# Performance work log

Hardware: AMD Instinct MI355X
Metric: run time of the kernel (lower is better)

## Reference

```python
import jax, jax.numpy as jnp
import numpy as np

DELTA_COEFF = 1.0
CLAMP_MIN = 1e-3  # hardcoded in original clamp(min=0.001)


def setup_inputs() -> dict:
    key = jax.random.key(0)
    k1, k2, k3 = jax.random.split(key, 3)
    B, N, F_in, F_out = 2, 1024, 128, 64
    x = jax.random.normal(k1, (B, N, F_in), dtype=jnp.float32)
    adj = jax.random.uniform(k2, (B, N, N), dtype=jnp.float32)
    weight = jax.random.normal(k3, (F_in, F_out), dtype=jnp.float32) * (1.0 / np.sqrt(F_in))
    bias = jnp.zeros((F_out,), dtype=jnp.float32)
    return {"x": x, "adj": adj, "weight": weight, "bias": bias}


def reference(x, adj, weight, bias):
    # x: [B,N,F_in], adj: [B,N,N]
    x = x @ weight  # [B,N,F_out]
    B, N, _ = adj.shape
    # pairwise L1 distance: [B,N,N]
    abs_diff = jnp.sum(jnp.abs(x[:, :, None, :] - x[:, None, :, :]), axis=-1)
    mod_adj = adj / jnp.maximum(abs_diff, CLAMP_MIN)
    deg = jnp.sum(mod_adj, axis=-1)  # [B,N]
    # Laplacian L = D - A~ ; then I - delta * L
    lap = jnp.zeros_like(mod_adj).at[:, jnp.arange(N), jnp.arange(N)].set(deg) - mod_adj
    mod = jnp.eye(N, dtype=x.dtype) - DELTA_COEFF * lap
    out = jnp.matmul(mod, x) + bias
    return out
```

## Files before the change

### kernel.cpp

```cpp
#include <hip/hip_runtime.h>
#include <hip/hip_fp16.h>


#define JS 16
#define HSTR 72

typedef _Float16 half8_t __attribute__((ext_vector_type(8)));
typedef _Float16 h2_t    __attribute__((ext_vector_type(2)));
typedef float    f32x4_t __attribute__((ext_vector_type(4)));

static __device__ __forceinline__ h2_t l1acc(h2_t acc, h2_t a, h2_t b) {
    h2_t d = a - b;
    unsigned ad = __builtin_bit_cast(unsigned, d) & 0x7FFF7FFFu;
    return acc + __builtin_bit_cast(h2_t, ad);
}

__global__ __launch_bounds__(256) void gemm_xw(const float* __restrict__ x,
                                               const float* __restrict__ w,
                                               float* __restrict__ xw,
                                               __half* __restrict__ xwh,
                                               __half* __restrict__ xwt) {
    __shared__ float ws_[128 * 64];
    __shared__ float xs[8 * 132];
    __shared__ __half ts[8 * 64];
    const int tid = threadIdx.x;
    const int r0  = blockIdx.x * 8;

#pragma unroll
    for (int e = tid; e < 2048; e += 256)
        ((float4*)ws_)[e] = ((const float4*)w)[e];
    {
        int row = tid >> 5, c = tid & 31;
        float4 v = *(const float4*)&x[(size_t)(r0 + row) * 128 + c * 4];
        *(float4*)&xs[row * 132 + c * 4] = v;
    }
    __syncthreads();

    const int rl = tid >> 5;
    const int fg = tid & 31;
    float2 acc = {0.f, 0.f};
#pragma unroll
    for (int k4 = 0; k4 < 32; ++k4) {
        float4 xv = *(const float4*)&xs[rl * 132 + k4 * 4];
        const float* xp = &xv.x;
#pragma unroll
        for (int m = 0; m < 4; ++m) {
            float2 wv = *(const float2*)&ws_[(k4 * 4 + m) * 64 + 2 * fg];
            acc.x += xp[m] * wv.x; acc.y += xp[m] * wv.y;
        }
    }
    size_t o = (size_t)(r0 + rl) * 64 + 2 * fg;
    *(float2*)&xw[o] = acc;
    __half2 h2 = __floats2half2_rn(acc.x, acc.y);
    *(__half2*)&xwh[o] = h2;
    *(__half2*)&ts[rl * 64 + 2 * fg] = h2;
    __syncthreads();

    if (tid < 64) {
        const int f = tid;
        const int b = r0 >> 10;
        const int n0 = r0 & 1023;
        __half hv[8];
#pragma unroll
        for (int r = 0; r < 8; ++r) hv[r] = ts[r * 64 + f];
        *(half8_t*)&xwt[((size_t)(b * 64 + f)) * 1024 + n0] = *(half8_t*)hv;
    }
}

template <bool ATOMIC>
__global__ __launch_bounds__(256) void fused_gtv(const __half* __restrict__ xwh,
                                                 const __half* __restrict__ xwt,
                                                 const float* __restrict__ adj,
                                                 __half* __restrict__ part,
                                                 float* __restrict__ aout,
                                                 float* __restrict__ pdeg) {
    __shared__ __half xih[32 * HSTR];
    __shared__ __half xjh[64 * HSTR];
    __shared__ __half xjt[64 * HSTR];
    __shared__ __half wt [32 * HSTR];

    const int tid = threadIdx.x;
    const int bx  = blockIdx.x;
    const int js  = bx & 15;
    const int it  = (bx >> 4) & 31;
    const int b   = bx >> 9;
    const int i0  = it * 32;
    const int j0  = js * 64;

    const __half* xhb = xwh + (size_t)b * 65536;
    const __half* xtb = xwt + (size_t)b * 65536;
    const float*  adjb = adj + (size_t)b * 1048576;

    const int ty = tid >> 4;
    const int tx = tid & 15;

    float4 av[2];
#pragma unroll
    for (int r = 0; r < 2; ++r)
        av[r] = *(const float4*)&adjb[(size_t)(i0 + 2 * ty + r) * 1024 + j0 + 4 * tx];

    {
        int row = tid >> 3, cb = tid & 7;
        int sc = ((cb ^ ((row >> 2) & 7)) << 3);
        float4 vi = *(const float4*)&xhb[(i0 + row) * 64 + cb * 8];
        *(float4*)&xih[row * HSTR + sc] = vi;
    }
#pragma unroll
    for (int e = tid; e < 512; e += 256) {
        int row = e >> 3, cb = e & 7;
        int sc = ((cb ^ ((row >> 2) & 7)) << 3);
        float4 vj = *(const float4*)&xhb[(j0 + row) * 64 + cb * 8];
        *(float4*)&xjh[row * HSTR + sc] = vj;
        float4 vt = *(const float4*)&xtb[row * 1024 + j0 + cb * 8];
        *(float4*)&xjt[row * HSTR + cb * 8] = vt;
    }
    __syncthreads();

    h2_t acc[2][4];
#pragma unroll
    for (int r = 0; r < 2; ++r)
#pragma unroll
        for (int q = 0; q < 4; ++q)
            acc[r][q] = (h2_t){(_Float16)0, (_Float16)0};

#pragma unroll
    for (int c = 0; c < 8; ++c) {
        const int ca = ((c ^ ((ty >> 1) & 7)) << 3);
        const int cb = ((c ^ (tx & 7)) << 3);
        float4 a[2], bb[4];
#pragma unroll
        for (int r = 0; r < 2; ++r)
            a[r] = *(const float4*)&xih[(2 * ty + r) * HSTR + ca];
#pragma unroll
        for (int q = 0; q < 4; ++q)
            bb[q] = *(const float4*)&xjh[(4 * tx + q) * HSTR + cb];
#pragma unroll
        for (int r = 0; r < 2; ++r) {
            const h2_t* pa = (const h2_t*)&a[r];
#pragma unroll
            for (int q = 0; q < 4; ++q) {
                const h2_t* pb = (const h2_t*)&bb[q];
#pragma unroll
                for (int m = 0; m < 4; ++m)
                    acc[r][q] = l1acc(acc[r][q], pa[m], pb[m]);
            }
        }
    }

    float dsum[2];
#pragma unroll
    for (int r = 0; r < 2; ++r) {
        const int gi = i0 + 2 * ty + r;
        float wv[4];
        dsum[r] = 0.f;
#pragma unroll
        for (int q = 0; q < 4; ++q) {
            float d = (float)acc[r][q][0] + (float)acc[r][q][1];
            float inv = __builtin_amdgcn_rcpf(fmaxf(d, 1e-3f));
            float v = (&av[r].x)[q] * inv;
            wv[q] = (gi == j0 + 4 * tx + q) ? 0.f : v;
            dsum[r] += wv[q];
        }
        float2 packed;
        ((__half2*)&packed)[0] = __floats2half2_rn(wv[0], wv[1]);
        ((__half2*)&packed)[1] = __floats2half2_rn(wv[2], wv[3]);
        *(float2*)&wt[(2 * ty + r) * HSTR + 4 * tx] = packed;
    }
#pragma unroll
    for (int r = 0; r < 2; ++r) {
#pragma unroll
        for (int m = 1; m < 16; m <<= 1)
            dsum[r] += __shfl_xor(dsum[r], m, 16);
    }
    if (tx == 0) {
#pragma unroll
        for (int r = 0; r < 2; ++r) {
            if (ATOMIC) atomicAdd(&pdeg[b * 1024 + i0 + 2 * ty + r], dsum[r]);
            else pdeg[(js * 2 + b) * 1024 + i0 + 2 * ty + r] = dsum[r];
        }
    }
    __syncthreads();

    const int wv_  = tid >> 6;
    const int lane = tid & 63;
    const int quad = lane >> 4;
    const int l15  = lane & 15;
    const int mt   = wv_ & 1;
    const int nb   = (wv_ >> 1) * 2;

    f32x4_t c[2] = {{0,0,0,0},{0,0,0,0}};
    half8_t a0 = *(half8_t*)&wt[(mt * 16 + l15) * HSTR + quad * 8];
    half8_t a1 = *(half8_t*)&wt[(mt * 16 + l15) * HSTR + 32 + quad * 8];
#pragma unroll
    for (int n = 0; n < 2; ++n) {
        half8_t b0 = *(half8_t*)&xjt[((nb + n) * 16 + l15) * HSTR + quad * 8];
        half8_t b1 = *(half8_t*)&xjt[((nb + n) * 16 + l15) * HSTR + 32 + quad * 8];
        c[n] = __builtin_amdgcn_mfma_f32_16x16x32_f16(a0, b0, c[n], 0, 0, 0);
        c[n] = __builtin_amdgcn_mfma_f32_16x16x32_f16(a1, b1, c[n], 0, 0, 0);
    }

    if (ATOMIC) {
#pragma unroll
        for (int n = 0; n < 2; ++n)
#pragma unroll
            for (int r = 0; r < 4; ++r) {
                int row = mt * 16 + quad * 4 + r;
                atomicAdd(&aout[((size_t)b * 1024 + i0 + row) * 64 + (nb + n) * 16 + l15], c[n][r]);
            }
    } else {
        const size_t slot = (size_t)(js * 2 + b) * 65536;
#pragma unroll
        for (int n = 0; n < 2; ++n)
#pragma unroll
            for (int r = 0; r < 4; ++r) {
                int row = mt * 16 + quad * 4 + r;
                part[slot + (i0 + row) * 64 + (nb + n) * 16 + l15] = __float2half(c[n][r]);
            }
    }
}

__global__ __launch_bounds__(256) void finish_gtv_v2(const float* __restrict__ xw,
                                                     const __half* __restrict__ part,
                                                     const float* __restrict__ pdeg,
                                                     const float* __restrict__ bias,
                                                     float* __restrict__ out) {
    int idx2 = blockIdx.x * 256 + threadIdx.x;
    int f2 = idx2 & 31;
    int r  = idx2 >> 5;
    int b  = r >> 10;
    int n  = r & 1023;

    float2 s = {0.f, 0.f};
    float dgs = 0.f;
    const __half2* p2 = (const __half2*)part;
#pragma unroll
    for (int js = 0; js < JS; ++js) {
        int sl = js * 2 + b;
        __half2 h = p2[(size_t)sl * 32768 + n * 32 + f2];
        float2 f = __half22float2(h);
        s.x += f.x; s.y += f.y;
        dgs += pdeg[sl * 1024 + n];
    }
    float2 xv = ((const float2*)xw)[idx2];
    float2 bv = ((const float2*)bias)[f2];
    float id = 1.f - dgs;
    float2 o;
    o.x = s.x + id * xv.x + bv.x;
    o.y = s.y + id * xv.y + bv.y;
    ((float2*)out)[idx2] = o;
}

__global__ __launch_bounds__(256) void finish_gtv_atomic(const float* __restrict__ xw,
                                                         const float* __restrict__ pdeg,
                                                         const float* __restrict__ bias,
                                                         float* __restrict__ out) {
    int idx = blockIdx.x * 256 + threadIdx.x;
    int f = idx & 63;
    int r = idx >> 6;
    out[idx] = out[idx] + (1.f - pdeg[r]) * xw[idx] + bias[f];
}

extern "C" void kernel_launch(void* const* d_in, const int* in_sizes, int n_in,
                              void* d_out, int out_size, void* d_ws, size_t ws_size,
                              hipStream_t stream) {
    const float* x    = (const float*)d_in[0];
    const float* adj  = (const float*)d_in[1];
    const float* w    = (const float*)d_in[2];
    const float* bias = (const float*)d_in[3];
    float* out = (float*)d_out;

    char* wsb = (char*)d_ws;
    float*  xw   = (float*)wsb;
    __half* xwh  = (__half*)(wsb + 512 * 1024);
    __half* xwt  = (__half*)(wsb + 768 * 1024);
    float*  pdeg = (float*)(wsb + 1024 * 1024);
    __half* part = (__half*)(wsb + 1152 * 1024);
    const size_t NEED = 1152 * 1024 + (size_t)32 * 65536 * 2;

    gemm_xw<<<256, 256, 0, stream>>>(x, w, xw, xwh, xwt);

    if (ws_size >= NEED) {
        fused_gtv<false><<<1024, 256, 0, stream>>>(xwh, xwt, adj, part, nullptr, pdeg);
        finish_gtv_v2<<<256, 256, 0, stream>>>(xw, part, pdeg, bias, out);
    } else {
        hipMemsetAsync(out, 0, 2 * 1024 * 64 * sizeof(float), stream);
        hipMemsetAsync(pdeg, 0, 2 * 1024 * sizeof(float), stream);
        fused_gtv<true><<<1024, 256, 0, stream>>>(xwh, xwt, adj, nullptr, out, pdeg);
        finish_gtv_atomic<<<512, 256, 0, stream>>>(xw, pdeg, bias, out);
    }
}
```

Before: 82.13 us.

## Process two j-tiles per block with register-prefetched double-buffered shared memory

Each fused block now handles two 64-column j-tiles instead of one, which halves the grid to 512 blocks and halves the number of partial slots written and then reduced by the finish kernel. The second tile's xw data is prefetched into registers while the first tile is computed, then stored into a second shared buffer. The intent is to reuse the i-tile across two j-tiles, cut the partial-sum traffic, and hide some of the global load latency. In exchange, shared memory use and register pressure per block go up and fewer blocks are available to fill the GPU.

```diff
diff --git a/kernel.cpp b/kernel.cpp
--- a/kernel.cpp
+++ b/kernel.cpp
@@ -2,7 +2,7 @@
 #include <hip/hip_fp16.h>
 
 
-#define JS 16
+#define JS 8
 #define HSTR 72
 
 typedef _Float16 half8_t __attribute__((ext_vector_type(8)));
@@ -75,17 +75,18 @@
                                                  float* __restrict__ aout,
                                                  float* __restrict__ pdeg) {
     __shared__ __half xih[32 * HSTR];
-    __shared__ __half xjh[64 * HSTR];
-    __shared__ __half xjt[64 * HSTR];
-    __shared__ __half wt [32 * HSTR];
+    __shared__ __half xjh[2][64 * HSTR];
+    __shared__ __half xjt[2][64 * HSTR];
+    __shared__ __half wt [2][32 * HSTR];
 
     const int tid = threadIdx.x;
     const int bx  = blockIdx.x;
-    const int js  = bx & 15;
-    const int it  = (bx >> 4) & 31;
-    const int b   = bx >> 9;
+    const int jg  = bx & 7;
+    const int it  = (bx >> 3) & 31;
+    const int b   = bx >> 8;
     const int i0  = it * 32;
-    const int j0  = js * 64;
+    const int jb0 = jg * 128;
+    const int jb1 = jb0 + 64;
 
     const __half* xhb = xwh + (size_t)b * 65536;
     const __half* xtb = xwt + (size_t)b * 65536;
@@ -94,92 +95,39 @@
     const int ty = tid >> 4;
     const int tx = tid & 15;
 
-    float4 av[2];
-#pragma unroll
-    for (int r = 0; r < 2; ++r)
-        av[r] = *(const float4*)&adjb[(size_t)(i0 + 2 * ty + r) * 1024 + j0 + 4 * tx];
+    float4 av[2][2];
+#pragma unroll
+    for (int t = 0; t < 2; ++t)
+#pragma unroll
+        for (int r = 0; r < 2; ++r)
+            av[t][r] = *(const float4*)&adjb[(size_t)(i0 + 2 * ty + r) * 1024 +
+                                             jb0 + t * 64 + 4 * tx];
 
     {
         int row = tid >> 3, cb = tid & 7;
         int sc = ((cb ^ ((row >> 2) & 7)) << 3);
-        float4 vi = *(const float4*)&xhb[(i0 + row) * 64 + cb * 8];
-        *(float4*)&xih[row * HSTR + sc] = vi;
+        *(float4*)&xih[row * HSTR + sc] =
+            *(const float4*)&xhb[(i0 + row) * 64 + cb * 8];
     }
 #pragma unroll
     for (int e = tid; e < 512; e += 256) {
         int row = e >> 3, cb = e & 7;
         int sc = ((cb ^ ((row >> 2) & 7)) << 3);
-        float4 vj = *(const float4*)&xhb[(j0 + row) * 64 + cb * 8];
-        *(float4*)&xjh[row * HSTR + sc] = vj;
-        float4 vt = *(const float4*)&xtb[row * 1024 + j0 + cb * 8];
-        *(float4*)&xjt[row * HSTR + cb * 8] = vt;
+        *(float4*)&xjh[0][row * HSTR + sc] =
+            *(const float4*)&xhb[(jb0 + row) * 64 + cb * 8];
+        *(float4*)&xjt[0][row * HSTR + cb * 8] =
+            *(const float4*)&xtb[row * 1024 + jb0 + cb * 8];
     }
     __syncthreads();
 
-    h2_t acc[2][4];
-#pragma unroll
-    for (int r = 0; r < 2; ++r)
-#pragma unroll
-        for (int q = 0; q < 4; ++q)
-            acc[r][q] = (h2_t){(_Float16)0, (_Float16)0};
-
-#pragma unroll
-    for (int c = 0; c < 8; ++c) {
-        const int ca = ((c ^ ((ty >> 1) & 7)) << 3);
-        const int cb = ((c ^ (tx & 7)) << 3);
-        float4 a[2], bb[4];
-#pragma unroll
-        for (int r = 0; r < 2; ++r)
-            a[r] = *(const float4*)&xih[(2 * ty + r) * HSTR + ca];
-#pragma unroll
-        for (int q = 0; q < 4; ++q)
-            bb[q] = *(const float4*)&xjh[(4 * tx + q) * HSTR + cb];
-#pragma unroll
-        for (int r = 0; r < 2; ++r) {
-            const h2_t* pa = (const h2_t*)&a[r];
-#pragma unroll
-            for (int q = 0; q < 4; ++q) {
-                const h2_t* pb = (const h2_t*)&bb[q];
-#pragma unroll
-                for (int m = 0; m < 4; ++m)
-                    acc[r][q] = l1acc(acc[r][q], pa[m], pb[m]);
-            }
-        }
-    }
-
-    float dsum[2];
-#pragma unroll
-    for (int r = 0; r < 2; ++r) {
-        const int gi = i0 + 2 * ty + r;
-        float wv[4];
-        dsum[r] = 0.f;
-#pragma unroll
-        for (int q = 0; q < 4; ++q) {
-            float d = (float)acc[r][q][0] + (float)acc[r][q][1];
-            float inv = __builtin_amdgcn_rcpf(fmaxf(d, 1e-3f));
-            float v = (&av[r].x)[q] * inv;
-            wv[q] = (gi == j0 + 4 * tx + q) ? 0.f : v;
-            dsum[r] += wv[q];
-        }
-        float2 packed;
-        ((__half2*)&packed)[0] = __floats2half2_rn(wv[0], wv[1]);
-        ((__half2*)&packed)[1] = __floats2half2_rn(wv[2], wv[3]);
-        *(float2*)&wt[(2 * ty + r) * HSTR + 4 * tx] = packed;
-    }
-#pragma unroll
-    for (int r = 0; r < 2; ++r) {
-#pragma unroll
-        for (int m = 1; m < 16; m <<= 1)
-            dsum[r] += __shfl_xor(dsum[r], m, 16);
-    }
-    if (tx == 0) {
-#pragma unroll
-        for (int r = 0; r < 2; ++r) {
-            if (ATOMIC) atomicAdd(&pdeg[b * 1024 + i0 + 2 * ty + r], dsum[r]);
-            else pdeg[(js * 2 + b) * 1024 + i0 + 2 * ty + r] = dsum[r];
-        }
-    }
-    __syncthreads();
+    float4 pj[2], pt[2];
+#pragma unroll
+    for (int k = 0; k < 2; ++k) {
+        int e = tid + k * 256;
+        int row = e >> 3, cb = e & 7;
+        pj[k] = *(const float4*)&xhb[(jb1 + row) * 64 + cb * 8];
+        pt[k] = *(const float4*)&xtb[row * 1024 + jb1 + cb * 8];
+    }
 
     const int wv_  = tid >> 6;
     const int lane = tid & 63;
@@ -188,15 +136,98 @@
     const int mt   = wv_ & 1;
     const int nb   = (wv_ >> 1) * 2;
 
+    float dsum[2] = {0.f, 0.f};
     f32x4_t c[2] = {{0,0,0,0},{0,0,0,0}};
-    half8_t a0 = *(half8_t*)&wt[(mt * 16 + l15) * HSTR + quad * 8];
-    half8_t a1 = *(half8_t*)&wt[(mt * 16 + l15) * HSTR + 32 + quad * 8];
-#pragma unroll
-    for (int n = 0; n < 2; ++n) {
-        half8_t b0 = *(half8_t*)&xjt[((nb + n) * 16 + l15) * HSTR + quad * 8];
-        half8_t b1 = *(half8_t*)&xjt[((nb + n) * 16 + l15) * HSTR + 32 + quad * 8];
-        c[n] = __builtin_amdgcn_mfma_f32_16x16x32_f16(a0, b0, c[n], 0, 0, 0);
-        c[n] = __builtin_amdgcn_mfma_f32_16x16x32_f16(a1, b1, c[n], 0, 0, 0);
+
+#pragma unroll
+    for (int t = 0; t < 2; ++t) {
+        const int jb = t ? jb1 : jb0;
+
+        h2_t acc[2][4];
+#pragma unroll
+        for (int r = 0; r < 2; ++r)
+#pragma unroll
+            for (int q = 0; q < 4; ++q)
+                acc[r][q] = (h2_t){(_Float16)0, (_Float16)0};
+
+#pragma unroll
+        for (int cc = 0; cc < 8; ++cc) {
+            const int ca = ((cc ^ ((ty >> 1) & 7)) << 3);
+            const int cb = ((cc ^ (tx & 7)) << 3);
+            float4 a[2], bb[4];
+#pragma unroll
+            for (int r = 0; r < 2; ++r)
+                a[r] = *(const float4*)&xih[(2 * ty + r) * HSTR + ca];
+#pragma unroll
+            for (int q = 0; q < 4; ++q)
+                bb[q] = *(const float4*)&xjh[t][(4 * tx + q) * HSTR + cb];
+#pragma unroll
+            for (int r = 0; r < 2; ++r) {
+                const h2_t* pa = (const h2_t*)&a[r];
+#pragma unroll
+                for (int q = 0; q < 4; ++q) {
+                    const h2_t* pb = (const h2_t*)&bb[q];
+#pragma unroll
+                    for (int m = 0; m < 4; ++m)
+                        acc[r][q] = l1acc(acc[r][q], pa[m], pb[m]);
+                }
+            }
+        }
+
+#pragma unroll
+        for (int r = 0; r < 2; ++r) {
+            const int gi = i0 + 2 * ty + r;
+            float wv[4];
+#pragma unroll
+            for (int q = 0; q < 4; ++q) {
+                float d = (float)acc[r][q][0] + (float)acc[r][q][1];
+                float inv = __builtin_amdgcn_rcpf(fmaxf(d, 1e-3f));
+                float v = (&av[t][r].x)[q] * inv;
+                wv[q] = (gi == jb + 4 * tx + q) ? 0.f : v;
+                dsum[r] += wv[q];
+            }
+            float2 packed;
+            ((__half2*)&packed)[0] = __floats2half2_rn(wv[0], wv[1]);
+            ((__half2*)&packed)[1] = __floats2half2_rn(wv[2], wv[3]);
+            *(float2*)&wt[t][(2 * ty + r) * HSTR + 4 * tx] = packed;
+        }
+        __syncthreads();
+
+        half8_t a0 = *(half8_t*)&wt[t][(mt * 16 + l15) * HSTR + quad * 8];
+        half8_t a1 = *(half8_t*)&wt[t][(mt * 16 + l15) * HSTR + 32 + quad * 8];
+#pragma unroll
+        for (int n = 0; n < 2; ++n) {
+            half8_t b0 = *(half8_t*)&xjt[t][((nb + n) * 16 + l15) * HSTR + quad * 8];
+            half8_t b1 = *(half8_t*)&xjt[t][((nb + n) * 16 + l15) * HSTR + 32 + quad * 8];
+            c[n] = __builtin_amdgcn_mfma_f32_16x16x32_f16(a0, b0, c[n], 0, 0, 0);
+            c[n] = __builtin_amdgcn_mfma_f32_16x16x32_f16(a1, b1, c[n], 0, 0, 0);
+        }
+
+        if (t == 0) {
+#pragma unroll
+            for (int k = 0; k < 2; ++k) {
+                int e = tid + k * 256;
+                int row = e >> 3, cb = e & 7;
+                int sc = ((cb ^ ((row >> 2) & 7)) << 3);
+                *(float4*)&xjh[1][row * HSTR + sc] = pj[k];
+                *(float4*)&xjt[1][row * HSTR + cb * 8] = pt[k];
+            }
+            __syncthreads();
+        }
+    }
+
+#pragma unroll
+    for (int r = 0; r < 2; ++r) {
+#pragma unroll
+        for (int m = 1; m < 16; m <<= 1)
+            dsum[r] += __shfl_xor(dsum[r], m, 16);
+    }
+    if (tx == 0) {
+#pragma unroll
+        for (int r = 0; r < 2; ++r) {
+            if (ATOMIC) atomicAdd(&pdeg[b * 1024 + i0 + 2 * ty + r], dsum[r]);
+            else pdeg[(jg * 2 + b) * 1024 + i0 + 2 * ty + r] = dsum[r];
+        }
     }
 
     if (ATOMIC) {
@@ -208,7 +239,7 @@
                 atomicAdd(&aout[((size_t)b * 1024 + i0 + row) * 64 + (nb + n) * 16 + l15], c[n][r]);
             }
     } else {
-        const size_t slot = (size_t)(js * 2 + b) * 65536;
+        const size_t slot = (size_t)(jg * 2 + b) * 65536;
 #pragma unroll
         for (int n = 0; n < 2; ++n)
 #pragma unroll
@@ -275,17 +306,17 @@
     __half* xwt  = (__half*)(wsb + 768 * 1024);
     float*  pdeg = (float*)(wsb + 1024 * 1024);
     __half* part = (__half*)(wsb + 1152 * 1024);
-    const size_t NEED = 1152 * 1024 + (size_t)32 * 65536 * 2;
+    const size_t NEED = 1152 * 1024 + (size_t)16 * 65536 * 2;
 
     gemm_xw<<<256, 256, 0, stream>>>(x, w, xw, xwh, xwt);
 
     if (ws_size >= NEED) {
-        fused_gtv<false><<<1024, 256, 0, stream>>>(xwh, xwt, adj, part, nullptr, pdeg);
+        fused_gtv<false><<<512, 256, 0, stream>>>(xwh, xwt, adj, part, nullptr, pdeg);
         finish_gtv_v2<<<256, 256, 0, stream>>>(xw, part, pdeg, bias, out);
     } else {
         hipMemsetAsync(out, 0, 2 * 1024 * 64 * sizeof(float), stream);
         hipMemsetAsync(pdeg, 0, 2 * 1024 * sizeof(float), stream);
-        fused_gtv<true><<<1024, 256, 0, stream>>>(xwh, xwt, adj, nullptr, out, pdeg);
+        fused_gtv<true><<<512, 256, 0, stream>>>(xwh, xwt, adj, nullptr, out, pdeg);
         finish_gtv_atomic<<<512, 256, 0, stream>>>(xw, pdeg, bias, out);
     }
 }
```

Measured after the change: 83.80 us. +2.0%, slower.

## Fuse x@W projection into the main pairwise kernel using MFMA recomputation

Applied to the files above, without the earlier changes.

Removes the separate gemm_xw launch. Each block of the main kernel now loads its 96 rows of x and all of W, converts them to fp16 and computes the projection with MFMA into shared memory, including the transposed copy. Blocks with js==0 also write the fp32 projection for the finish kernel. This saves one launch and the round trip of the intermediate through global memory. In exchange, every block redundantly recomputes the projection, rereads W from global memory with strided scalar loads, and uses much more shared memory, which may lower occupancy.

```diff
diff --git a/kernel.cpp b/kernel.cpp
--- a/kernel.cpp
+++ b/kernel.cpp
@@ -6,6 +6,7 @@
 #define HSTR 72
 
 typedef _Float16 half8_t __attribute__((ext_vector_type(8)));
+typedef _Float16 half4_t __attribute__((ext_vector_type(4)));
 typedef _Float16 h2_t    __attribute__((ext_vector_type(2)));
 typedef float    f32x4_t __attribute__((ext_vector_type(4)));
 
@@ -15,69 +16,20 @@
     return acc + __builtin_bit_cast(h2_t, ad);
 }
 
-__global__ __launch_bounds__(256) void gemm_xw(const float* __restrict__ x,
-                                               const float* __restrict__ w,
-                                               float* __restrict__ xw,
-                                               __half* __restrict__ xwh,
-                                               __half* __restrict__ xwt) {
-    __shared__ float ws_[128 * 64];
-    __shared__ float xs[8 * 132];
-    __shared__ __half ts[8 * 64];
-    const int tid = threadIdx.x;
-    const int r0  = blockIdx.x * 8;
-
-#pragma unroll
-    for (int e = tid; e < 2048; e += 256)
-        ((float4*)ws_)[e] = ((const float4*)w)[e];
-    {
-        int row = tid >> 5, c = tid & 31;
-        float4 v = *(const float4*)&x[(size_t)(r0 + row) * 128 + c * 4];
-        *(float4*)&xs[row * 132 + c * 4] = v;
-    }
-    __syncthreads();
-
-    const int rl = tid >> 5;
-    const int fg = tid & 31;
-    float2 acc = {0.f, 0.f};
-#pragma unroll
-    for (int k4 = 0; k4 < 32; ++k4) {
-        float4 xv = *(const float4*)&xs[rl * 132 + k4 * 4];
-        const float* xp = &xv.x;
-#pragma unroll
-        for (int m = 0; m < 4; ++m) {
-            float2 wv = *(const float2*)&ws_[(k4 * 4 + m) * 64 + 2 * fg];
-            acc.x += xp[m] * wv.x; acc.y += xp[m] * wv.y;
-        }
-    }
-    size_t o = (size_t)(r0 + rl) * 64 + 2 * fg;
-    *(float2*)&xw[o] = acc;
-    __half2 h2 = __floats2half2_rn(acc.x, acc.y);
-    *(__half2*)&xwh[o] = h2;
-    *(__half2*)&ts[rl * 64 + 2 * fg] = h2;
-    __syncthreads();
-
-    if (tid < 64) {
-        const int f = tid;
-        const int b = r0 >> 10;
-        const int n0 = r0 & 1023;
-        __half hv[8];
-#pragma unroll
-        for (int r = 0; r < 8; ++r) hv[r] = ts[r * 64 + f];
-        *(half8_t*)&xwt[((size_t)(b * 64 + f)) * 1024 + n0] = *(half8_t*)hv;
-    }
-}
-
 template <bool ATOMIC>
-__global__ __launch_bounds__(256) void fused_gtv(const __half* __restrict__ xwh,
-                                                 const __half* __restrict__ xwt,
+__global__ __launch_bounds__(256) void fused_all(const float* __restrict__ x,
+                                                 const float* __restrict__ w,
                                                  const float* __restrict__ adj,
                                                  __half* __restrict__ part,
                                                  float* __restrict__ aout,
-                                                 float* __restrict__ pdeg) {
-    __shared__ __half xih[32 * HSTR];
-    __shared__ __half xjh[64 * HSTR];
-    __shared__ __half xjt[64 * HSTR];
-    __shared__ __half wt [32 * HSTR];
+                                                 float* __restrict__ pdeg,
+                                                 float* __restrict__ xw) {
+    __shared__ __attribute__((aligned(16))) __half x16s[96 * 128];
+    __shared__ __attribute__((aligned(16))) __half wTs [64 * 128];
+    __shared__ __attribute__((aligned(16))) __half xih[32 * HSTR];
+    __shared__ __attribute__((aligned(16))) __half xjh[64 * HSTR];
+    __shared__ __attribute__((aligned(16))) __half xjt[64 * HSTR];
+    __half* const wt = x16s;
 
     const int tid = threadIdx.x;
     const int bx  = blockIdx.x;
@@ -87,9 +39,8 @@
     const int i0  = it * 32;
     const int j0  = js * 64;
 
-    const __half* xhb = xwh + (size_t)b * 65536;
-    const __half* xtb = xwt + (size_t)b * 65536;
-    const float*  adjb = adj + (size_t)b * 1048576;
+    const float* xb   = x + (size_t)b * 131072;
+    const float* adjb = adj + (size_t)b * 1048576;
 
     const int ty = tid >> 4;
     const int tx = tid & 15;
@@ -99,20 +50,84 @@
     for (int r = 0; r < 2; ++r)
         av[r] = *(const float4*)&adjb[(size_t)(i0 + 2 * ty + r) * 1024 + j0 + 4 * tx];
 
+#pragma unroll
+    for (int e = tid; e < 1536; e += 256) {
+        int row = e >> 4, c8 = e & 15;
+        int gr  = (row < 32) ? (i0 + row) : (j0 + row - 32);
+        const float* xp = &xb[(size_t)gr * 128 + c8 * 8];
+        float4 v0 = *(const float4*)xp;
+        float4 v1 = *(const float4*)(xp + 4);
+        _Float16 h[8];
+        h[0] = (_Float16)v0.x; h[1] = (_Float16)v0.y;
+        h[2] = (_Float16)v0.z; h[3] = (_Float16)v0.w;
+        h[4] = (_Float16)v1.x; h[5] = (_Float16)v1.y;
+        h[6] = (_Float16)v1.z; h[7] = (_Float16)v1.w;
+        *(half8_t*)&x16s[row * 128 + ((c8 ^ (row & 7)) << 3)] = *(half8_t*)h;
+    }
+#pragma unroll
+    for (int e = tid; e < 1024; e += 256) {
+        int f = e & 63, c8 = e >> 6;
+        _Float16 h[8];
+#pragma unroll
+        for (int m = 0; m < 8; ++m)
+            h[m] = (_Float16)w[(c8 * 8 + m) * 64 + f];
+        *(half8_t*)&wTs[f * 128 + ((c8 ^ (f & 7)) << 3)] = *(half8_t*)h;
+    }
+    __syncthreads();
+
+    const int wv_  = tid >> 6;
+    const int lane = tid & 63;
+    const int quad = lane >> 4;
+    const int l15  = lane & 15;
+
+    f32x4_t cxw[6];
+#pragma unroll
+    for (int rt = 0; rt < 6; ++rt) {
+        f32x4_t cc = {0.f, 0.f, 0.f, 0.f};
+#pragma unroll
+        for (int kc = 0; kc < 4; ++kc) {
+            int ch = ((kc * 4 + quad) ^ (l15 & 7)) << 3;
+            half8_t af = *(half8_t*)&x16s[(rt * 16 + l15) * 128 + ch];
+            half8_t bf = *(half8_t*)&wTs [(wv_ * 16 + l15) * 128 + ch];
+            cc = __builtin_amdgcn_mfma_f32_16x16x32_f16(af, bf, cc, 0, 0, 0);
+        }
+        cxw[rt] = cc;
+    }
+
     {
-        int row = tid >> 3, cb = tid & 7;
-        int sc = ((cb ^ ((row >> 2) & 7)) << 3);
-        float4 vi = *(const float4*)&xhb[(i0 + row) * 64 + cb * 8];
-        *(float4*)&xih[row * HSTR + sc] = vi;
-    }
-#pragma unroll
-    for (int e = tid; e < 512; e += 256) {
-        int row = e >> 3, cb = e & 7;
-        int sc = ((cb ^ ((row >> 2) & 7)) << 3);
-        float4 vj = *(const float4*)&xhb[(j0 + row) * 64 + cb * 8];
-        *(float4*)&xjh[row * HSTR + sc] = vj;
-        float4 vt = *(const float4*)&xtb[row * 1024 + j0 + cb * 8];
-        *(float4*)&xjt[row * HSTR + cb * 8] = vt;
+        const int f  = wv_ * 16 + l15;
+        const int cb = f >> 3;
+#pragma unroll
+        for (int rt = 0; rt < 2; ++rt) {
+#pragma unroll
+            for (int r = 0; r < 4; ++r) {
+                int lr = rt * 16 + quad * 4 + r;
+                xih[lr * HSTR + ((cb ^ ((lr >> 2) & 7)) << 3) + (f & 7)] =
+                    __float2half(cxw[rt][r]);
+            }
+        }
+#pragma unroll
+        for (int rt = 2; rt < 6; ++rt) {
+            _Float16 h4[4];
+#pragma unroll
+            for (int r = 0; r < 4; ++r) {
+                int jl = (rt - 2) * 16 + quad * 4 + r;
+                __half hv = __float2half(cxw[rt][r]);
+                xjh[jl * HSTR + ((cb ^ ((jl >> 2) & 7)) << 3) + (f & 7)] = hv;
+                h4[r] = *(_Float16*)&hv;
+            }
+            int jl0 = (rt - 2) * 16 + quad * 4;
+            *(half4_t*)&xjt[f * HSTR + jl0] = *(half4_t*)h4;
+        }
+        if (js == 0) {
+#pragma unroll
+            for (int rt = 0; rt < 2; ++rt)
+#pragma unroll
+                for (int r = 0; r < 4; ++r) {
+                    int lr = rt * 16 + quad * 4 + r;
+                    xw[((size_t)b * 1024 + i0 + lr) * 64 + f] = cxw[rt][r];
+                }
+        }
     }
     __syncthreads();
 
@@ -181,12 +196,8 @@
     }
     __syncthreads();
 
-    const int wv_  = tid >> 6;
-    const int lane = tid & 63;
-    const int quad = lane >> 4;
-    const int l15  = lane & 15;
-    const int mt   = wv_ & 1;
-    const int nb   = (wv_ >> 1) * 2;
+    const int mt = wv_ & 1;
+    const int nb = (wv_ >> 1) * 2;
 
     f32x4_t c[2] = {{0,0,0,0},{0,0,0,0}};
     half8_t a0 = *(half8_t*)&wt[(mt * 16 + l15) * HSTR + quad * 8];
@@ -271,21 +282,17 @@
 
     char* wsb = (char*)d_ws;
     float*  xw   = (float*)wsb;
-    __half* xwh  = (__half*)(wsb + 512 * 1024);
-    __half* xwt  = (__half*)(wsb + 768 * 1024);
     float*  pdeg = (float*)(wsb + 1024 * 1024);
     __half* part = (__half*)(wsb + 1152 * 1024);
     const size_t NEED = 1152 * 1024 + (size_t)32 * 65536 * 2;
 
-    gemm_xw<<<256, 256, 0, stream>>>(x, w, xw, xwh, xwt);
-
     if (ws_size >= NEED) {
-        fused_gtv<false><<<1024, 256, 0, stream>>>(xwh, xwt, adj, part, nullptr, pdeg);
+        fused_all<false><<<1024, 256, 0, stream>>>(x, w, adj, part, nullptr, pdeg, xw);
         finish_gtv_v2<<<256, 256, 0, stream>>>(xw, part, pdeg, bias, out);
     } else {
         hipMemsetAsync(out, 0, 2 * 1024 * 64 * sizeof(float), stream);
         hipMemsetAsync(pdeg, 0, 2 * 1024 * sizeof(float), stream);
-        fused_gtv<true><<<1024, 256, 0, stream>>>(xwh, xwt, adj, nullptr, out, pdeg);
+        fused_all<true><<<1024, 256, 0, stream>>>(x, w, adj, nullptr, out, pdeg, xw);
         finish_gtv_atomic<<<512, 256, 0, stream>>>(xw, pdeg, bias, out);
     }
 }
```

After: 82.86 us. About the same (+0.9%).
